# Kernel tuning notes

Measured on AMD Instinct MI355X. Metric: run time of the kernel, lower is better.

The kernel has to match this reference:

```python
import jax, jax.numpy as jnp
import numpy as np

B, T, C, H = 16, 2048, 1024, 64

def setup_inputs() -> dict:
    key = jax.random.key(0)
    kx, kq, kk, kv = jax.random.split(key, 4)
    s = 0.02
    return {
        "x": jax.random.normal(kx, (B, T, C), dtype=jnp.float32),
        "Wq": jax.random.normal(kq, (C, H), dtype=jnp.float32) * s,
        "Wk": jax.random.normal(kk, (C, H), dtype=jnp.float32) * s,
        "Wv": jax.random.normal(kv, (C, H), dtype=jnp.float32) * s,
    }

def reference(x, Wq, Wk, Wv):
    Bc, Tc, Cc = x.shape
    q = x @ Wq  # [B,T,H]
    k = x @ Wk  # [B,T,H]
    v = x @ Wv  # [B,T,H]
    # NOTE: original scales by n_embed^{-0.5} (C), not head_size^{-0.5}
    wei = jnp.einsum("bth,bsh->bts", q, k) * (Cc ** -0.5)  # [B,T,T]
    causal = jnp.tril(jnp.ones((Tc, Tc), dtype=bool))
    wei = jnp.where(causal, wei, -jnp.inf)
    wei = jax.nn.softmax(wei, axis=-1)
    # dropout is identity in eval mode
    out = jnp.einsum("bts,bsh->bth", wei, v)  # [B,T,H]
    return out
```

## Files before the change

### kernel.cpp

```cpp
#include <hip/hip_runtime.h>

typedef __attribute__((ext_vector_type(8))) short short8;
typedef __attribute__((ext_vector_type(4))) float float4v;

__device__ inline short f2bf(float f) {
    union { float f; unsigned int u; } c; c.f = f;
    unsigned int u = c.u;
    unsigned int r = (u + 0x7fffu + ((u >> 16) & 1u)) >> 16;
    return (short)r;
}

__device__ inline short8 pack8(float4 a, float4 b) {
    short8 r;
    r[0]=f2bf(a.x); r[1]=f2bf(a.y); r[2]=f2bf(a.z); r[3]=f2bf(a.w);
    r[4]=f2bf(b.x); r[5]=f2bf(b.y); r[6]=f2bf(b.z); r[7]=f2bf(b.w);
    return r;
}

__device__ inline void gl2lds16(const short* g, short* l) {
    __builtin_amdgcn_global_load_lds(
        (const __attribute__((address_space(1))) unsigned int*)g,
        (__attribute__((address_space(3))) unsigned int*)l, 16, 0, 0);
}


__global__ __launch_bounds__(256) void wconv_kernel(
    const float* __restrict__ Wq, const float* __restrict__ Wk,
    const float* __restrict__ Wv, short* __restrict__ Wt)
{
    __shared__ short Ls[64 * 72];
    const int w  = blockIdx.x >> 4;
    const int c  = blockIdx.x & 15;
    const int k0 = c * 64;
    const float* W = (w == 0) ? Wq : (w == 1) ? Wk : Wv;
    const int tid = threadIdx.x;

#pragma unroll
    for (int i = 0; i < 4; i++) {
        int kk = (tid >> 4) + i * 16;
        int c4 = (tid & 15) * 4;
        float4 v = *(const float4*)&W[(size_t)(k0 + kk) * 64 + c4];
        Ls[kk * 72 + c4 + 0] = f2bf(v.x);
        Ls[kk * 72 + c4 + 1] = f2bf(v.y);
        Ls[kk * 72 + c4 + 2] = f2bf(v.z);
        Ls[kk * 72 + c4 + 3] = f2bf(v.w);
    }
    __syncthreads();
    const int n  = tid >> 2;
    const int k8 = (tid & 3) * 16;
    short8 o0, o1;
#pragma unroll
    for (int j = 0; j < 8; j++) o0[j] = Ls[(k8 + j) * 72 + n];
#pragma unroll
    for (int j = 0; j < 8; j++) o1[j] = Ls[(k8 + 8 + j) * 72 + n];
    const int gn = w * 64 + n;
    short* base = &Wt[(size_t)gn * 1024 + k0 + k8];
    *(short8*)&base[0] = o0;
    *(short8*)&base[8] = o1;
}

__global__ __launch_bounds__(256) void qkv_kernel(
    const float* __restrict__ x, const short* __restrict__ Wt,
    short* __restrict__ qo, short* __restrict__ k_s, short* __restrict__ vT_t)
{
    const int tid  = threadIdx.x;
    const int wave = tid >> 6, lane = tid & 63;
    const int quad = lane >> 4, l16 = lane & 15;
    const int msub = wave >> 1;
    const int nh   = wave & 1;
    const int m0   = blockIdx.x * 64 + msub * 32;
    const int nc0  = nh * 96;

    const float* xr0 = &x[(size_t)(m0 + l16) * 1024 + quad * 8];
    const float* xr1 = xr0 + 16 * 1024;
    const short* wp  = &Wt[(size_t)(nc0 + l16) * 1024 + quad * 8];

    float4v acc[2][6];
#pragma unroll
    for (int mf = 0; mf < 2; mf++)
#pragma unroll
        for (int nt = 0; nt < 6; nt++) acc[mf][nt] = (float4v)0.0f;

    float4 n0 = *(const float4*)(xr0);
    float4 n1 = *(const float4*)(xr0 + 4);
    float4 n2 = *(const float4*)(xr0 + 32);
    float4 n3 = *(const float4*)(xr0 + 36);
    float4 n4 = *(const float4*)(xr1);
    float4 n5 = *(const float4*)(xr1 + 4);
    float4 n6 = *(const float4*)(xr1 + 32);
    float4 n7 = *(const float4*)(xr1 + 36);

    for (int s = 0; s < 16; s++) {
        short8 af00 = pack8(n0, n1);
        short8 af01 = pack8(n2, n3);
        short8 af10 = pack8(n4, n5);
        short8 af11 = pack8(n6, n7);
        if (s < 15) {
            const float* p0 = xr0 + (size_t)(s + 1) * 64;
            const float* p1 = xr1 + (size_t)(s + 1) * 64;
            n0 = *(const float4*)(p0);      n1 = *(const float4*)(p0 + 4);
            n2 = *(const float4*)(p0 + 32); n3 = *(const float4*)(p0 + 36);
            n4 = *(const float4*)(p1);      n5 = *(const float4*)(p1 + 4);
            n6 = *(const float4*)(p1 + 32); n7 = *(const float4*)(p1 + 36);
        }
        const short* wk = wp + s * 64;
#pragma unroll
        for (int nt = 0; nt < 6; nt++) {
            short8 bf = *(const short8*)(wk + (size_t)nt * 16 * 1024);
            acc[0][nt] = __builtin_amdgcn_mfma_f32_16x16x32_bf16(af00, bf, acc[0][nt], 0, 0, 0);
            acc[1][nt] = __builtin_amdgcn_mfma_f32_16x16x32_bf16(af10, bf, acc[1][nt], 0, 0, 0);
        }
#pragma unroll
        for (int nt = 0; nt < 6; nt++) {
            short8 bf = *(const short8*)(wk + 32 + (size_t)nt * 16 * 1024);
            acc[0][nt] = __builtin_amdgcn_mfma_f32_16x16x32_bf16(af01, bf, acc[0][nt], 0, 0, 0);
            acc[1][nt] = __builtin_amdgcn_mfma_f32_16x16x32_bf16(af11, bf, acc[1][nt], 0, 0, 0);
        }
    }

#pragma unroll
    for (int mf = 0; mf < 2; mf++) {
#pragma unroll
        for (int nt = 0; nt < 6; nt++) {
            int g = nc0 + nt * 16 + l16;
#pragma unroll
            for (int r = 0; r < 4; r++) {
                int row = m0 + mf * 16 + quad * 4 + r;
                short val = f2bf(acc[mf][nt][r]);
                if (g < 64) {
                    qo[(size_t)row * 64 + g] = val;
                } else if (g < 128) {
                    int h = g - 64;
                    k_s[(size_t)row * 64 + (((h >> 3) ^ (row & 7)) * 8 + (h & 7))] = val;
                } else {
                    int h = g - 128;
                    int bb = row >> 11, tt = row & 2047;
                    int tc = tt >> 6, tl = tt & 63;
                    vT_t[(((size_t)bb * 32 + tc) * 64 + h) * 64 +
                         (((tl >> 3) ^ (h & 7)) * 8 + (tl & 7))] = val;
                }
            }
        }
    }
}

#define SCALE_LOG2E 0.04508422132f

__global__ __launch_bounds__(256) void attn_kernel(
    const short* __restrict__ q, const short* __restrict__ k_s,
    const short* __restrict__ vT_t, float* __restrict__ out)
{
    __shared__ short Ks[2][64 * 64];
    __shared__ short Vs[2][64 * 64];
    __shared__ short Ps[64 * 72];

    const int tid  = threadIdx.x;
    const int wave = tid >> 6, lane = tid & 63;
    const int quad = lane >> 4, l16 = lane & 15;

    int b, qt;
    if (blockIdx.x < 256) { b = blockIdx.x >> 4; qt = 16 + (blockIdx.x & 15); }
    else { int t2 = blockIdx.x - 256; b = t2 >> 4; qt = 15 - (t2 & 15); }

    const short* kb = k_s  + (size_t)b * 2048 * 64;
    const short* vb = vT_t + (size_t)b * 32 * 64 * 64;

    const short* qrow = q + ((size_t)b * 2048 + qt*64 + wave*16 + l16) * 64;
    short8 qf0 = *(const short8*)&qrow[quad*8];
    short8 qf1 = *(const short8*)&qrow[32 + quad*8];

    float4v oacc[4];
#pragma unroll
    for (int t = 0; t < 4; t++) oacc[t] = (float4v)0.0f;
    float l_i[4] = {0.f, 0.f, 0.f, 0.f};

    const int tg   = qt*64 + wave*16 + quad*4;
    const int jmax = qt;
    const int lofs = lane * 8;

    {
        const short* kg = kb + ((size_t)wave * 16) * 64;
        short* kl = &Ks[0][wave * 16 * 64];
        gl2lds16(kg +       lofs, kl +       lofs);
        gl2lds16(kg + 512 + lofs, kl + 512 + lofs);
        const short* vg = vb + ((size_t)wave * 16) * 64;
        short* vl = &Vs[0][wave * 16 * 64];
        gl2lds16(vg +       lofs, vl +       lofs);
        gl2lds16(vg + 512 + lofs, vl + 512 + lofs);
    }
    __syncthreads();

    int cur = 0;
    for (int j = 0; j <= jmax; j++) {
        const int nxt = cur ^ 1;
        if (j < jmax) {
            const short* kg = kb + ((size_t)(j + 1) * 64 + wave * 16) * 64;
            short* kl = &Ks[nxt][wave * 16 * 64];
            gl2lds16(kg +       lofs, kl +       lofs);
            gl2lds16(kg + 512 + lofs, kl + 512 + lofs);
            const short* vg = vb + ((size_t)(j + 1) * 64 + wave * 16) * 64;
            short* vl = &Vs[nxt][wave * 16 * 64];
            gl2lds16(vg +       lofs, vl +       lofs);
            gl2lds16(vg + 512 + lofs, vl + 512 + lofs);
        }
        const short* Ksc = Ks[cur];
        const short* Vsc = Vs[cur];

        float4v sacc[4];
#pragma unroll
        for (int t = 0; t < 4; t++) sacc[t] = (float4v)0.0f;
#pragma unroll
        for (int t = 0; t < 4; t++) {
            int brow = t*16 + l16;
            short8 b0 = *(const short8*)&Ksc[brow * 64 + ((    quad) ^ (brow & 7)) * 8];
            short8 b1 = *(const short8*)&Ksc[brow * 64 + ((4 + quad) ^ (brow & 7)) * 8];
            sacc[t] = __builtin_amdgcn_mfma_f32_16x16x32_bf16(qf0, b0, sacc[t], 0, 0, 0);
            sacc[t] = __builtin_amdgcn_mfma_f32_16x16x32_bf16(qf1, b1, sacc[t], 0, 0, 0);
        }
        if (j == jmax) {
#pragma unroll
            for (int t = 0; t < 4; t++) {
                int sg = j*64 + t*16 + l16;
#pragma unroll
                for (int r = 0; r < 4; r++) {
                    float p = exp2f(sacc[t][r] * SCALE_LOG2E);
                    if (sg > tg + r) p = 0.0f;
                    sacc[t][r] = p;
                    l_i[r] += p;
                }
            }
        } else {
#pragma unroll
            for (int t = 0; t < 4; t++)
#pragma unroll
                for (int r = 0; r < 4; r++) {
                    float p = exp2f(sacc[t][r] * SCALE_LOG2E);
                    sacc[t][r] = p;
                    l_i[r] += p;
                }
        }
#pragma unroll
        for (int t = 0; t < 4; t++)
#pragma unroll
            for (int r = 0; r < 4; r++)
                Ps[(wave*16 + quad*4 + r) * 72 + t*16 + l16] = f2bf(sacc[t][r]);
#pragma unroll
        for (int kc = 0; kc < 2; kc++) {
            short8 af = *(const short8*)&Ps[(wave*16 + l16) * 72 + kc*32 + quad*8];
#pragma unroll
            for (int t = 0; t < 4; t++) {
                int drow = t*16 + l16;
                short8 bf = *(const short8*)&Vsc[drow * 64 + ((kc*4 + quad) ^ (drow & 7)) * 8];
                oacc[t] = __builtin_amdgcn_mfma_f32_16x16x32_bf16(af, bf, oacc[t], 0, 0, 0);
            }
        }
        __syncthreads();
        cur = nxt;
    }
#pragma unroll
    for (int off = 1; off < 16; off <<= 1)
#pragma unroll
        for (int r = 0; r < 4; r++)
            l_i[r] += __shfl_xor(l_i[r], off, 64);
#pragma unroll
    for (int r = 0; r < 4; r++) {
        float inv = 1.0f / l_i[r];
        int row = qt*64 + wave*16 + quad*4 + r;
#pragma unroll
        for (int t = 0; t < 4; t++)
            out[((size_t)b * 2048 + row) * 64 + t*16 + l16] = oacc[t][r] * inv;
    }
}

extern "C" void kernel_launch(void* const* d_in, const int* in_sizes, int n_in,
                              void* d_out, int out_size, void* d_ws, size_t ws_size,
                              hipStream_t stream)
{
    const float* x  = (const float*)d_in[0];
    const float* Wq = (const float*)d_in[1];
    const float* Wk = (const float*)d_in[2];
    const float* Wv = (const float*)d_in[3];

    short* qw   = (short*)d_ws;
    short* ks   = qw + (size_t)32768 * 64;
    short* vTt  = ks + (size_t)32768 * 64;
    short* Wts  = vTt + (size_t)32768 * 64;
    float* out  = (float*)d_out;

    hipLaunchKernelGGL(wconv_kernel, dim3(48), dim3(256), 0, stream,
                       Wq, Wk, Wv, Wts);
    hipLaunchKernelGGL(qkv_kernel, dim3(512), dim3(256), 0, stream,
                       x, Wts, qw, ks, vTt);
    hipLaunchKernelGGL(attn_kernel, dim3(512), dim3(256), 0, stream,
                       qw, ks, vTt, out);
}
```

Before: 282.1 us.

## Pre-swizzle weights into MFMA fragment order and retile QKV projection across waves

The weight conversion kernel now writes bf16 weights directly in MFMA B-fragment order, so each lane's operand is a contiguous coalesced 16-byte load instead of a strided row read. The QKV projection is retiled so each block covers 32 rows with four waves each owning 48 output columns, which doubles the grid and halves per-wave accumulators. A launch bound of four blocks per CU is added, and the float-to-bf16 packing uses the hardware v_cvt_pk_bf16_f32 instruction instead of manual rounding. The cost is that every x row tile is now loaded by all four waves instead of two, which doubles x traffic through L2.

```diff
diff --git a/kernel.cpp b/kernel.cpp
--- a/kernel.cpp
+++ b/kernel.cpp
@@ -10,11 +10,13 @@
     return (short)r;
 }
 
-__device__ inline short8 pack8(float4 a, float4 b) {
-    short8 r;
-    r[0]=f2bf(a.x); r[1]=f2bf(a.y); r[2]=f2bf(a.z); r[3]=f2bf(a.w);
-    r[4]=f2bf(b.x); r[5]=f2bf(b.y); r[6]=f2bf(b.z); r[7]=f2bf(b.w);
-    return r;
+__device__ inline short8 pack8_cvt(float4 a, float4 b) {
+    union { short8 s; unsigned int u[4]; } r;
+    asm("v_cvt_pk_bf16_f32 %0, %1, %2" : "=v"(r.u[0]) : "v"(a.x), "v"(a.y));
+    asm("v_cvt_pk_bf16_f32 %0, %1, %2" : "=v"(r.u[1]) : "v"(a.z), "v"(a.w));
+    asm("v_cvt_pk_bf16_f32 %0, %1, %2" : "=v"(r.u[2]) : "v"(b.x), "v"(b.y));
+    asm("v_cvt_pk_bf16_f32 %0, %1, %2" : "=v"(r.u[3]) : "v"(b.z), "v"(b.w));
+    return r.s;
 }
 
 __device__ inline void gl2lds16(const short* g, short* l) {
@@ -26,60 +28,49 @@
 
 __global__ __launch_bounds__(256) void wconv_kernel(
     const float* __restrict__ Wq, const float* __restrict__ Wk,
-    const float* __restrict__ Wv, short* __restrict__ Wt)
-{
-    __shared__ short Ls[64 * 72];
-    const int w  = blockIdx.x >> 4;
-    const int c  = blockIdx.x & 15;
-    const int k0 = c * 64;
-    const float* W = (w == 0) ? Wq : (w == 1) ? Wk : Wv;
+    const float* __restrict__ Wv, short* __restrict__ Wt_f)
+{
+    const int s   = blockIdx.x;
     const int tid = threadIdx.x;
-
-#pragma unroll
-    for (int i = 0; i < 4; i++) {
-        int kk = (tid >> 4) + i * 16;
-        int c4 = (tid & 15) * 4;
-        float4 v = *(const float4*)&W[(size_t)(k0 + kk) * 64 + c4];
-        Ls[kk * 72 + c4 + 0] = f2bf(v.x);
-        Ls[kk * 72 + c4 + 1] = f2bf(v.y);
-        Ls[kk * 72 + c4 + 2] = f2bf(v.z);
-        Ls[kk * 72 + c4 + 3] = f2bf(v.w);
-    }
-    __syncthreads();
-    const int n  = tid >> 2;
-    const int k8 = (tid & 3) * 16;
-    short8 o0, o1;
-#pragma unroll
-    for (int j = 0; j < 8; j++) o0[j] = Ls[(k8 + j) * 72 + n];
-#pragma unroll
-    for (int j = 0; j < 8; j++) o1[j] = Ls[(k8 + 8 + j) * 72 + n];
-    const int gn = w * 64 + n;
-    short* base = &Wt[(size_t)gn * 1024 + k0 + k8];
-    *(short8*)&base[0] = o0;
-    *(short8*)&base[8] = o1;
-}
-
-__global__ __launch_bounds__(256) void qkv_kernel(
-    const float* __restrict__ x, const short* __restrict__ Wt,
+#pragma unroll
+    for (int i = 0; i < 6; i++) {
+        int idx  = tid + i * 256;
+        int lane = idx & 63;
+        int c    = idx >> 6;
+        int kc2  = c & 1;
+        int nt   = (c >> 1) % 3;
+        int w    = c / 6;
+        int g    = w * 48 + nt * 16 + (lane & 15);
+        const float* W = (g < 64) ? Wq : (g < 128) ? Wk : Wv;
+        int col   = g & 63;
+        int kbase = s * 64 + kc2 * 32 + (lane >> 4) * 8;
+        short8 o;
+#pragma unroll
+        for (int j = 0; j < 8; j++)
+            o[j] = f2bf(W[(size_t)(kbase + j) * 64 + col]);
+        *(short8*)&Wt_f[((size_t)s * 1536 + idx) * 8] = o;
+    }
+}
+
+__global__ __launch_bounds__(256, 4) void qkv_kernel(
+    const float* __restrict__ x, const short* __restrict__ Wt_f,
     short* __restrict__ qo, short* __restrict__ k_s, short* __restrict__ vT_t)
 {
     const int tid  = threadIdx.x;
     const int wave = tid >> 6, lane = tid & 63;
     const int quad = lane >> 4, l16 = lane & 15;
-    const int msub = wave >> 1;
-    const int nh   = wave & 1;
-    const int m0   = blockIdx.x * 64 + msub * 32;
-    const int nc0  = nh * 96;
+    const int m0   = blockIdx.x * 32;
+    const int nc0  = wave * 48;
 
     const float* xr0 = &x[(size_t)(m0 + l16) * 1024 + quad * 8];
     const float* xr1 = xr0 + 16 * 1024;
-    const short* wp  = &Wt[(size_t)(nc0 + l16) * 1024 + quad * 8];
-
-    float4v acc[2][6];
+    const short* bp0 = &Wt_f[((size_t)wave * 384 + lane) * 8];
+
+    float4v acc[2][3];
 #pragma unroll
     for (int mf = 0; mf < 2; mf++)
 #pragma unroll
-        for (int nt = 0; nt < 6; nt++) acc[mf][nt] = (float4v)0.0f;
+        for (int nt = 0; nt < 3; nt++) acc[mf][nt] = (float4v)0.0f;
 
     float4 n0 = *(const float4*)(xr0);
     float4 n1 = *(const float4*)(xr0 + 4);
@@ -91,10 +82,10 @@
     float4 n7 = *(const float4*)(xr1 + 36);
 
     for (int s = 0; s < 16; s++) {
-        short8 af00 = pack8(n0, n1);
-        short8 af01 = pack8(n2, n3);
-        short8 af10 = pack8(n4, n5);
-        short8 af11 = pack8(n6, n7);
+        short8 af00 = pack8_cvt(n0, n1);
+        short8 af01 = pack8_cvt(n2, n3);
+        short8 af10 = pack8_cvt(n4, n5);
+        short8 af11 = pack8_cvt(n6, n7);
         if (s < 15) {
             const float* p0 = xr0 + (size_t)(s + 1) * 64;
             const float* p1 = xr1 + (size_t)(s + 1) * 64;
@@ -103,25 +94,22 @@
             n4 = *(const float4*)(p1);      n5 = *(const float4*)(p1 + 4);
             n6 = *(const float4*)(p1 + 32); n7 = *(const float4*)(p1 + 36);
         }
-        const short* wk = wp + s * 64;
-#pragma unroll
-        for (int nt = 0; nt < 6; nt++) {
-            short8 bf = *(const short8*)(wk + (size_t)nt * 16 * 1024);
-            acc[0][nt] = __builtin_amdgcn_mfma_f32_16x16x32_bf16(af00, bf, acc[0][nt], 0, 0, 0);
-            acc[1][nt] = __builtin_amdgcn_mfma_f32_16x16x32_bf16(af10, bf, acc[1][nt], 0, 0, 0);
-        }
-#pragma unroll
-        for (int nt = 0; nt < 6; nt++) {
-            short8 bf = *(const short8*)(wk + 32 + (size_t)nt * 16 * 1024);
-            acc[0][nt] = __builtin_amdgcn_mfma_f32_16x16x32_bf16(af01, bf, acc[0][nt], 0, 0, 0);
-            acc[1][nt] = __builtin_amdgcn_mfma_f32_16x16x32_bf16(af11, bf, acc[1][nt], 0, 0, 0);
+        const short* bp = bp0 + (size_t)s * 12288;
+#pragma unroll
+        for (int nt = 0; nt < 3; nt++) {
+            short8 bf0 = *(const short8*)(bp + nt * 1024);
+            short8 bf1 = *(const short8*)(bp + nt * 1024 + 512);
+            acc[0][nt] = __builtin_amdgcn_mfma_f32_16x16x32_bf16(af00, bf0, acc[0][nt], 0, 0, 0);
+            acc[1][nt] = __builtin_amdgcn_mfma_f32_16x16x32_bf16(af10, bf0, acc[1][nt], 0, 0, 0);
+            acc[0][nt] = __builtin_amdgcn_mfma_f32_16x16x32_bf16(af01, bf1, acc[0][nt], 0, 0, 0);
+            acc[1][nt] = __builtin_amdgcn_mfma_f32_16x16x32_bf16(af11, bf1, acc[1][nt], 0, 0, 0);
         }
     }
 
 #pragma unroll
     for (int mf = 0; mf < 2; mf++) {
 #pragma unroll
-        for (int nt = 0; nt < 6; nt++) {
+        for (int nt = 0; nt < 3; nt++) {
             int g = nc0 + nt * 16 + l16;
 #pragma unroll
             for (int r = 0; r < 4; r++) {
@@ -284,13 +272,13 @@
     short* qw   = (short*)d_ws;
     short* ks   = qw + (size_t)32768 * 64;
     short* vTt  = ks + (size_t)32768 * 64;
-    short* Wts  = vTt + (size_t)32768 * 64;
+    short* Wtf  = vTt + (size_t)32768 * 64;
     float* out  = (float*)d_out;
 
-    hipLaunchKernelGGL(wconv_kernel, dim3(48), dim3(256), 0, stream,
-                       Wq, Wk, Wv, Wts);
-    hipLaunchKernelGGL(qkv_kernel, dim3(512), dim3(256), 0, stream,
-                       x, Wts, qw, ks, vTt);
+    hipLaunchKernelGGL(wconv_kernel, dim3(16), dim3(256), 0, stream,
+                       Wq, Wk, Wv, Wtf);
+    hipLaunchKernelGGL(qkv_kernel, dim3(1024), dim3(256), 0, stream,
+                       x, Wtf, qw, ks, vTt);
     hipLaunchKernelGGL(attn_kernel, dim3(512), dim3(256), 0, stream,
                        qw, ks, vTt, out);
 }
```

Result: no change. 286.2 us (+1.5%).
